# Kernel tuning notes

Measured on AMD Instinct MI355X. Metric: run time of the kernel, lower is better.

The kernel has to match this reference:

```python
import math
import jax, jax.numpy as jnp
import numpy as np

B, T, S = 4, 1024, 1024
D, H, V = 512, 8, 32000
DK = D // H
PAD_ID = 0


def _layernorm(x, g, b, eps=1e-5):
    mu = jnp.mean(x, axis=-1, keepdims=True)
    var = jnp.mean((x - mu) ** 2, axis=-1, keepdims=True)
    return g * (x - mu) / jnp.sqrt(var + eps) + b


def _pos_encoding(t, d, dtype):
    pos = jnp.arange(t, dtype=jnp.float32)[:, None]
    freqs = 1.0 / (10000.0 ** (jnp.arange(0, d, 2, dtype=jnp.float32) / d))
    pe = jnp.zeros((t, d), jnp.float32)
    pe = pe.at[:, 0::2].set(jnp.sin(pos * freqs))
    pe = pe.at[:, 1::2].set(jnp.cos(pos * freqs))
    return pe.astype(dtype)


def _split_heads(x):  # [B,L,D] -> [B,H,L,DK]
    b, l, _ = x.shape
    return x.reshape(b, l, H, DK).transpose(0, 2, 1, 3)


def _merge_heads(x):  # [B,H,L,DK] -> [B,L,D]
    b, h, l, dk = x.shape
    return x.transpose(0, 2, 1, 3).reshape(b, l, h * dk)


def _attn(q, k, v, mask):  # mask True = blocked, broadcastable to [B,H,Tq,Tk]
    s = jnp.einsum('bhqd,bhkd->bhqk', q, k) / math.sqrt(DK)
    s = jnp.where(mask, jnp.finfo(s.dtype).min, s)
    a = jax.nn.softmax(s, axis=-1)
    return jnp.einsum('bhqk,bhkd->bhqd', a, v)


def setup_inputs() -> dict:
    key = jax.random.key(0)
    ks = iter(jax.random.split(key, 40))
    def W(o, i):
        return jax.random.normal(next(ks), (o, i), jnp.float32) * 0.02
    def bvec(o):
        return jnp.zeros((o,), jnp.float32)
    inp = {
        'tokens': jax.random.randint(next(ks), (B, T), 0, V),
        'enc_embeddings': jax.random.normal(next(ks), (B, S, D), jnp.float32),
        'enc_pad_mask': jnp.zeros((B, S), bool),
        'emb': jax.random.normal(next(ks), (V, D), jnp.float32) * 0.02,
        'Wq': W(D, D), 'bq': bvec(D), 'Wk': W(D, D), 'bk': bvec(D),
        'Wv': W(D, D), 'bv': bvec(D), 'Wo1': W(D, D), 'bo1': bvec(D),
        'cWq': W(D, D), 'cbq': bvec(D), 'eWk': W(D, D), 'ebk': bvec(D),
        'eWv': W(D, D), 'ebv': bvec(D), 'Wo2': W(D, D), 'bo2': bvec(D),
        'W1': W(2 * D, D), 'b1': bvec(2 * D), 'W2': W(D, 2 * D), 'b2': bvec(D),
        'g1': jnp.ones((D,), jnp.float32), 'be1': bvec(D),
        'g2': jnp.ones((D,), jnp.float32), 'be2': bvec(D),
        'g3': jnp.ones((D,), jnp.float32), 'be3': bvec(D),
        'Wout': W(V, D), 'bout': bvec(V),
    }
    return inp


def reference(tokens, enc_embeddings, enc_pad_mask, emb,
              Wq, bq, Wk, bk, Wv, bv, Wo1, bo1,
              cWq, cbq, eWk, ebk, eWv, ebv, Wo2, bo2,
              W1, b1, W2, b2, g1, be1, g2, be2, g3, be3, Wout, bout):
    lin = lambda x, w, b: x @ w.T + b
    x = emb[tokens] * math.sqrt(D)                      # [B,T,D]
    x = x + _pos_encoding(T, D, x.dtype)[None]
    # causal self-attention with key-padding mask
    q = _split_heads(lin(x, Wq, bq))
    k = _split_heads(lin(x, Wk, bk))
    v = _split_heads(lin(x, Wv, bv))
    causal = jnp.arange(T)[None, :] > jnp.arange(T)[:, None]          # [T,T]
    key_pad = (tokens == PAD_ID)[:, None, None, :]                    # [B,1,1,T]
    sa = _merge_heads(_attn(q, k, v, causal[None, None] | key_pad))
    x = _layernorm(lin(sa, Wo1, bo1) + x, g1, be1)
    # cross-attention
    dq = _split_heads(lin(x, cWq, cbq))
    ek = _split_heads(lin(enc_embeddings, eWk, ebk))
    ev = _split_heads(lin(enc_embeddings, eWv, ebv))
    ca = _merge_heads(_attn(dq, ek, ev, enc_pad_mask[:, None, None, :]))
    x = _layernorm(lin(ca, Wo2, bo2) + x, g3, be3)
    # FFN
    fp = lin(jax.nn.relu(lin(x, W1, b1)), W2, b2)
    x = _layernorm(x + fp, g2, be2)
    return lin(x, Wout, bout)                            # [B,T,V]
```

## Files before the change

### kernel.cpp

```cpp
#include <hip/hip_runtime.h>

#define DEV __device__ __forceinline__

typedef unsigned short u16;
typedef __attribute__((ext_vector_type(8))) __bf16 bf16x8;
typedef __attribute__((ext_vector_type(4))) float f32x4;

DEV u16 f2b(float f) {
    unsigned u = __builtin_bit_cast(unsigned, f);
    unsigned r = u + 0x7fffu + ((u >> 16) & 1u);
    return (u16)(r >> 16);
}

DEV f32x4 mfma16(bf16x8 a, bf16x8 b, f32x4 c) {
    return __builtin_amdgcn_mfma_f32_16x16x32_bf16(a, b, c, 0, 0, 0);
}

#define GLOAD_LDS16(gp, lp)                                                       \
    __builtin_amdgcn_global_load_lds((__attribute__((address_space(1))) void*)(gp), \
                                     (__attribute__((address_space(3))) void*)(lp), \
                                     16, 0, 0)

template <int L>
DEV void wait_ring(int kt, int NT) {
    if (kt + 2 < NT) {
        if constexpr (L == 2) asm volatile("s_waitcnt vmcnt(4)" ::: "memory");
        if constexpr (L == 3) asm volatile("s_waitcnt vmcnt(6)" ::: "memory");
        if constexpr (L == 4) asm volatile("s_waitcnt vmcnt(8)" ::: "memory");
    } else if (kt + 1 < NT) {
        if constexpr (L == 2) asm volatile("s_waitcnt vmcnt(2)" ::: "memory");
        if constexpr (L == 3) asm volatile("s_waitcnt vmcnt(3)" ::: "memory");
        if constexpr (L == 4) asm volatile("s_waitcnt vmcnt(4)" ::: "memory");
    } else {
        asm volatile("s_waitcnt vmcnt(0)" ::: "memory");
    }
}

struct CastArgs {
    const float4* src[12];
    ushort4* dst[12];
    int start4[13];
    const int* tokens;
    const float* emb;
    float* xf;
    u16* xb;
};

__global__ __launch_bounds__(256) void cast_embed_k(CastArgs a) {
    const int bid = blockIdx.x;
    if (bid < 4096) {
        int i   = bid * 256 + threadIdx.x;
        int row = i >> 8;
        int dp  = i & 255;
        int pos = row & 1023;
        int tok = a.tokens[row];
        const float* e = a.emb + (size_t)tok * 512 + dp * 2;
        float e0 = e[0] * 22.627416997969522f;
        float e1 = e[1] * 22.627416997969522f;
        float freq = exp2f(-(float)dp * 0.05190512648262190f);
        float ang  = (float)pos * freq;
        float v0 = e0 + __sinf(ang);
        float v1 = e1 + __cosf(ang);
        size_t o = (size_t)row * 512 + dp * 2;
        a.xf[o] = v0; a.xf[o + 1] = v1;
        a.xb[o] = f2b(v0); a.xb[o + 1] = f2b(v1);
        return;
    }
    const int total = a.start4[12];
    const int nblk = gridDim.x - 4096;
    for (int i = (bid - 4096) * 256 + threadIdx.x; i < total; i += nblk * 256) {
        int j = 0;
#pragma unroll
        for (int t = 1; t < 12; t++) j += (i >= a.start4[t]) ? 1 : 0;
        const int loc = i - a.start4[j];
        float4 v = a.src[j][loc];
        ushort4 o;
        o.x = f2b(v.x); o.y = f2b(v.y); o.z = f2b(v.z); o.w = f2b(v.w);
        a.dst[j][loc] = o;
    }
}

template <int BM, int BN>
__global__ __launch_bounds__(256) void gemm_sm_k(const u16* __restrict__ A,
                                                 const u16* __restrict__ W,
                                                 const float* __restrict__ b0,
                                                 const float* __restrict__ b1,
                                                 const float* __restrict__ b2,
                                                 float* __restrict__ Cf,
                                                 u16* __restrict__ Cb,
                                                 int M, int N, int K, int relu) {
    constexpr int MF = BM / 32;
    constexpr int NF = BN / 32;
    constexpr int CH_A = BM * 4;
    constexpr int CH_TOT = (BM + BN) * 4;
    constexpr int L = CH_TOT / 256;
    __shared__ u16 sA[4][BM * 32];
    __shared__ u16 sB[4][BN * 32];

    const int gx = gridDim.x;
    const int nwg = gx * gridDim.y;
    const int orig = blockIdx.y * gx + blockIdx.x;
    const int xcd = orig & 7, chnk = orig >> 3;
    const int q = nwg >> 3, r = nwg & 7;
    const int wgid = (xcd < r ? xcd * (q + 1) : r * (q + 1) + (xcd - r) * q) + chnk;
    const int m0 = (wgid % gx) * BM;
    const int n0 = (wgid / gx) * BN;

    const int tid  = threadIdx.x;
    const int lane = tid & 63;
    const int wid  = tid >> 6;
    const int wr = wid >> 1, wc = wid & 1;
    const int lg = lane >> 4, lr = lane & 15;

    f32x4 acc[MF][NF];
#pragma unroll
    for (int i = 0; i < MF; i++)
#pragma unroll
        for (int j = 0; j < NF; j++) acc[i][j] = (f32x4){0.f, 0.f, 0.f, 0.f};

    auto stage = [&](int b, int kt) {
        const int k0 = kt << 5;
#pragma unroll
        for (int h = 0; h < L; h++) {
            const int c = tid + h * 256;
            if (c < CH_A) {
                const int row = c >> 2, ch = c & 3;
                const int gch = ch ^ ((row >> 1) & 3);
                GLOAD_LDS16(A + (size_t)(m0 + row) * K + k0 + gch * 8,
                            &sA[b][c * 8]);
            } else {
                const int cb = c - CH_A;
                const int row = cb >> 2, ch = cb & 3;
                const int gch = ch ^ ((row >> 1) & 3);
                GLOAD_LDS16(W + (size_t)(n0 + row) * K + k0 + gch * 8,
                            &sB[b][cb * 8]);
            }
        }
    };

    const int NT = K >> 5;
    stage(0, 0); stage(1, 1); stage(2, 2);

    for (int kt = 0; kt < NT; kt++) {
        wait_ring<L>(kt, NT);
        __builtin_amdgcn_s_barrier();
        const int bsel = kt & 3;
        if (kt + 3 < NT) stage((kt + 3) & 3, kt + 3);

        bf16x8 af[MF], bfr[NF];
#pragma unroll
        for (int mi = 0; mi < MF; mi++) {
            const int row = wr * (BM / 2) + mi * 16 + lr;
            af[mi] = *(const bf16x8*)(&sA[bsel][row * 32 + (lg ^ ((row >> 1) & 3)) * 8]);
        }
#pragma unroll
        for (int ni = 0; ni < NF; ni++) {
            const int row = wc * (BN / 2) + ni * 16 + lr;
            bfr[ni] = *(const bf16x8*)(&sB[bsel][row * 32 + (lg ^ ((row >> 1) & 3)) * 8]);
        }
        __builtin_amdgcn_s_setprio(1);
#pragma unroll
        for (int mi = 0; mi < MF; mi++)
#pragma unroll
            for (int ni = 0; ni < NF; ni++)
                acc[mi][ni] = mfma16(af[mi], bfr[ni], acc[mi][ni]);
        __builtin_amdgcn_s_setprio(0);
    }

#pragma unroll
    for (int mi = 0; mi < MF; mi++) {
        const int rbase = m0 + wr * (BM / 2) + mi * 16 + lg * 4;
#pragma unroll
        for (int ni = 0; ni < NF; ni++) {
            const int col = n0 + wc * (BN / 2) + ni * 16 + lr;
            const float* bp = b0; int cc = col;
            if (b1 && col >= 512)  { bp = b1; cc = col - 512; }
            if (b2 && col >= 1024) { bp = b2; cc = col - 1024; }
            const float bv = bp[cc];
#pragma unroll
            for (int rr = 0; rr < 4; rr++) {
                float v = acc[mi][ni][rr] + bv;
                if (relu) v = fmaxf(v, 0.f);
                if (Cf) Cf[(size_t)(rbase + rr) * N + col] = v;
                if (Cb) Cb[(size_t)(rbase + rr) * N + col] = f2b(v);
            }
        }
    }
}

__global__ __launch_bounds__(256) void gemm_wout_k(const u16* __restrict__ A,
                                                   const u16* __restrict__ W,
                                                   const float* __restrict__ bias,
                                                   float* __restrict__ C,
                                                   int M, int N, int K) {
    __shared__ u16 sA[2][128 * 32];
    __shared__ u16 sB[2][128 * 32];
    const int orig = blockIdx.x;
    const int wgid = (orig & 7) * (8000 / 8) + (orig >> 3);
    const int m0 = (wgid & 31) * 128;
    const int n0 = (wgid >> 5) * 128;

    const int tid  = threadIdx.x;
    const int lane = tid & 63;
    const int wid  = tid >> 6;
    const int wr = wid >> 1, wc = wid & 1;
    const int lg = lane >> 4, lr = lane & 15;

    f32x4 acc[4][4];
#pragma unroll
    for (int i = 0; i < 4; i++)
#pragma unroll
        for (int j = 0; j < 4; j++) acc[i][j] = (f32x4){0.f, 0.f, 0.f, 0.f};

    auto stage = [&](int b, int kt) {
        const int k0 = kt << 5;
#pragma unroll
        for (int h = 0; h < 4; h++) {
            const int c = tid + h * 256;
            if (c < 512) {
                const int row = c >> 2, ch = c & 3;
                const int gch = ch ^ ((row >> 1) & 3);
                GLOAD_LDS16(A + (size_t)(m0 + row) * K + k0 + gch * 8,
                            &sA[b][c * 8]);
            } else {
                const int cb = c - 512;
                const int row = cb >> 2, ch = cb & 3;
                const int gch = ch ^ ((row >> 1) & 3);
                GLOAD_LDS16(W + (size_t)(n0 + row) * K + k0 + gch * 8,
                            &sB[b][cb * 8]);
            }
        }
    };

    const int NT = K >> 5;
    stage(0, 0);
    for (int kt = 0; kt < NT; kt++) {
        asm volatile("s_waitcnt vmcnt(0)" ::: "memory");
        __builtin_amdgcn_s_barrier();
        const int bsel = kt & 1;
        if (kt + 1 < NT) stage(bsel ^ 1, kt + 1);

        bf16x8 af[4], bfr[4];
#pragma unroll
        for (int mi = 0; mi < 4; mi++) {
            const int row = wr * 64 + mi * 16 + lr;
            af[mi] = *(const bf16x8*)(&sA[bsel][row * 32 + (lg ^ ((row >> 1) & 3)) * 8]);
        }
#pragma unroll
        for (int ni = 0; ni < 4; ni++) {
            const int row = wc * 64 + ni * 16 + lr;
            bfr[ni] = *(const bf16x8*)(&sB[bsel][row * 32 + (lg ^ ((row >> 1) & 3)) * 8]);
        }
        __builtin_amdgcn_s_setprio(1);
#pragma unroll
        for (int mi = 0; mi < 4; mi++)
#pragma unroll
            for (int ni = 0; ni < 4; ni++)
                acc[mi][ni] = mfma16(af[mi], bfr[ni], acc[mi][ni]);
        __builtin_amdgcn_s_setprio(0);
    }

#pragma unroll
    for (int mi = 0; mi < 4; mi++) {
        const int rbase = m0 + wr * 64 + mi * 16 + lg * 4;
#pragma unroll
        for (int ni = 0; ni < 4; ni++) {
            const int col = n0 + wc * 64 + ni * 16 + lr;
            const float bv = bias[col];
#pragma unroll
            for (int rr = 0; rr < 4; rr++)
                __builtin_nontemporal_store(acc[mi][ni][rr] + bv,
                                            &C[(size_t)(rbase + rr) * N + col]);
        }
    }
}

struct DualArgs {
    const u16 *A0, *W0, *A1, *W1;
    const float *b00, *b01, *b02, *b10, *b11;
    u16 *C0, *C1;
};

__global__ __launch_bounds__(256) void gemm_dual_k(DualArgs da) {
    constexpr int BM = 64, BN = 128, MF = 2, NF = 4;
    constexpr int CH_A = BM * 4, CH_TOT = (BM + BN) * 4, L = CH_TOT / 256;
    __shared__ u16 sA[4][BM * 32];
    __shared__ u16 sB[4][BN * 32];

    const int z = blockIdx.z;
    const int gy = z ? 8 : 12;
    if ((int)blockIdx.y >= gy) return;
    const int N = z ? 1024 : 1536;
    const u16* A = z ? da.A1 : da.A0;
    const u16* W = z ? da.W1 : da.W0;
    u16* C = z ? da.C1 : da.C0;
    const int K = 512;

    const int gx = gridDim.x;
    const int nwg = gx * gy;
    const int orig = blockIdx.y * gx + blockIdx.x;
    const int xcd = orig & 7, chnk = orig >> 3;
    const int q = nwg >> 3, r = nwg & 7;
    const int wgid = (xcd < r ? xcd * (q + 1) : r * (q + 1) + (xcd - r) * q) + chnk;
    const int m0 = (wgid % gx) * BM;
    const int n0 = (wgid / gx) * BN;

    const int tid  = threadIdx.x;
    const int lane = tid & 63;
    const int wid  = tid >> 6;
    const int wr = wid >> 1, wc = wid & 1;
    const int lg = lane >> 4, lr = lane & 15;

    f32x4 acc[MF][NF];
#pragma unroll
    for (int i = 0; i < MF; i++)
#pragma unroll
        for (int j = 0; j < NF; j++) acc[i][j] = (f32x4){0.f, 0.f, 0.f, 0.f};

    auto stage = [&](int b, int kt) {
        const int k0 = kt << 5;
#pragma unroll
        for (int h = 0; h < L; h++) {
            const int c = tid + h * 256;
            if (c < CH_A) {
                const int row = c >> 2, ch = c & 3;
                const int gch = ch ^ ((row >> 1) & 3);
                GLOAD_LDS16(A + (size_t)(m0 + row) * K + k0 + gch * 8,
                            &sA[b][c * 8]);
            } else {
                const int cb = c - CH_A;
                const int row = cb >> 2, ch = cb & 3;
                const int gch = ch ^ ((row >> 1) & 3);
                GLOAD_LDS16(W + (size_t)(n0 + row) * K + k0 + gch * 8,
                            &sB[b][cb * 8]);
            }
        }
    };

    const int NT = K >> 5;
    stage(0, 0); stage(1, 1); stage(2, 2);

    for (int kt = 0; kt < NT; kt++) {
        wait_ring<L>(kt, NT);
        __builtin_amdgcn_s_barrier();
        const int bsel = kt & 3;
        if (kt + 3 < NT) stage((kt + 3) & 3, kt + 3);

        bf16x8 af[MF], bfr[NF];
#pragma unroll
        for (int mi = 0; mi < MF; mi++) {
            const int row = wr * (BM / 2) + mi * 16 + lr;
            af[mi] = *(const bf16x8*)(&sA[bsel][row * 32 + (lg ^ ((row >> 1) & 3)) * 8]);
        }
#pragma unroll
        for (int ni = 0; ni < NF; ni++) {
            const int row = wc * (BN / 2) + ni * 16 + lr;
            bfr[ni] = *(const bf16x8*)(&sB[bsel][row * 32 + (lg ^ ((row >> 1) & 3)) * 8]);
        }
        __builtin_amdgcn_s_setprio(1);
#pragma unroll
        for (int mi = 0; mi < MF; mi++)
#pragma unroll
            for (int ni = 0; ni < NF; ni++)
                acc[mi][ni] = mfma16(af[mi], bfr[ni], acc[mi][ni]);
        __builtin_amdgcn_s_setprio(0);
    }

#pragma unroll
    for (int mi = 0; mi < MF; mi++) {
        const int rbase = m0 + wr * (BM / 2) + mi * 16 + lg * 4;
#pragma unroll
        for (int ni = 0; ni < NF; ni++) {
            const int col = n0 + wc * (BN / 2) + ni * 16 + lr;
            const float* bp; int cc;
            if (z == 0) {
                if (col >= 1024)     { bp = da.b02; cc = col - 1024; }
                else if (col >= 512) { bp = da.b01; cc = col - 512; }
                else                 { bp = da.b00; cc = col; }
            } else {
                if (col >= 512)      { bp = da.b11; cc = col - 512; }
                else                 { bp = da.b10; cc = col; }
            }
            const float bv = bp[cc];
#pragma unroll
            for (int rr = 0; rr < 4; rr++)
                C[(size_t)(rbase + rr) * N + col] = f2b(acc[mi][ni][rr] + bv);
        }
    }
}

__global__ __launch_bounds__(256) void vt_k(const u16* __restrict__ V0, int rs0,
                                            u16* __restrict__ VT0,
                                            const u16* __restrict__ V1, int rs1,
                                            u16* __restrict__ VT1) {
    const u16* V = blockIdx.z ? V1 : V0;
    u16* VT = blockIdx.z ? VT1 : VT0;
    const int rs = blockIdx.z ? rs1 : rs0;
    const int bh = blockIdx.x;
    const int b = bh >> 3;
    const int h64 = (bh & 7) * 64;
    const int t0 = blockIdx.y * 64;
    __shared__ u16 s[64 * 65];
    const int tid = threadIdx.x;
#pragma unroll
    for (int i = 0; i < 16; i++) {
        int t = (tid >> 6) + i * 4;
        int d = tid & 63;
        s[d * 65 + t] = V[(size_t)(b * 1024 + t0 + t) * rs + h64 + d];
    }
    __syncthreads();
#pragma unroll
    for (int i = 0; i < 16; i++) {
        int d = (tid >> 6) + i * 4;
        int t = tid & 63;
        VT[(size_t)(bh * 64 + d) * 1024 + t0 + t] = s[d * 65 + t];
    }
}

template <int CAUSAL>
__global__ __launch_bounds__(64) void attn_k(const u16* __restrict__ Q, int qrs,
                                             const u16* __restrict__ Kb, int krs,
                                             const u16* __restrict__ VT,
                                             const int* __restrict__ tokens,
                                             const signed char* __restrict__ km8,
                                             u16* __restrict__ O, int LK) {
    const int bh = blockIdx.x;
    const int b = bh >> 3;
    const int h64 = (bh & 7) * 64;
    const int qb = blockIdx.y;
    const int lane = threadIdx.x;
    const int lg = lane >> 4, lr = lane & 15;
    const float NEG = -3.402823466e38f;

    const u16* qrow = Q + (size_t)(b * 1024 + qb * 16 + lr) * qrs + h64 + lg * 8;
    const bf16x8 aq0 = *(const bf16x8*)(qrow);
    const bf16x8 aq1 = *(const bf16x8*)(qrow + 32);

    f32x4 o[4];
#pragma unroll
    for (int ni = 0; ni < 4; ni++) o[ni] = (f32x4){0.f, 0.f, 0.f, 0.f};
    float m_run[4], l_run[4];
#pragma unroll
    for (int rr = 0; rr < 4; rr++) { m_run[rr] = NEG; l_run[rr] = 0.f; }

    __shared__ u16 sP[16 * 72];
    const u16* vbase = VT + (size_t)bh * 64 * LK;

    auto body = [&](int k0) {
        f32x4 s[4];
#pragma unroll
        for (int c = 0; c < 4; c++) {
            const u16* krow =
                Kb + (size_t)(b * LK + k0 + c * 16 + lr) * krs + h64 + lg * 8;
            bf16x8 bk0 = *(const bf16x8*)(krow);
            bf16x8 bk1 = *(const bf16x8*)(krow + 32);
            f32x4 t = (f32x4){0.f, 0.f, 0.f, 0.f};
            t = mfma16(aq0, bk0, t);
            t = mfma16(aq1, bk1, t);
            s[c] = t;
        }
#pragma unroll
        for (int c = 0; c < 4; c++) {
            const int key = k0 + c * 16 + lr;
            bool mkey;
            if (CAUSAL) mkey = (tokens[b * LK + key] == 0);
            else        mkey = (km8[b * LK + key] != 0);
#pragma unroll
            for (int rr = 0; rr < 4; rr++) {
                float sv = s[c][rr] * 0.125f;
                bool mk = mkey;
                if (CAUSAL) mk = mk || (key > qb * 16 + lg * 4 + rr);
                s[c][rr] = mk ? NEG : sv;
            }
        }
        float pf[4];
#pragma unroll
        for (int rr = 0; rr < 4; rr++) {
            float bm = fmaxf(fmaxf(s[0][rr], s[1][rr]), fmaxf(s[2][rr], s[3][rr]));
            bm = fmaxf(bm, __shfl_xor(bm, 1));
            bm = fmaxf(bm, __shfl_xor(bm, 2));
            bm = fmaxf(bm, __shfl_xor(bm, 4));
            bm = fmaxf(bm, __shfl_xor(bm, 8));
            float mn = fmaxf(m_run[rr], bm);
            float sc = __expf(m_run[rr] - mn);
            float p0 = __expf(s[0][rr] - mn);
            float p1 = __expf(s[1][rr] - mn);
            float p2 = __expf(s[2][rr] - mn);
            float p3 = __expf(s[3][rr] - mn);
            float bs = (p0 + p1) + (p2 + p3);
            bs += __shfl_xor(bs, 1);
            bs += __shfl_xor(bs, 2);
            bs += __shfl_xor(bs, 4);
            bs += __shfl_xor(bs, 8);
            l_run[rr] = l_run[rr] * sc + bs;
            m_run[rr] = mn;
            pf[rr] = sc;
            s[0][rr] = p0; s[1][rr] = p1; s[2][rr] = p2; s[3][rr] = p3;
        }
#pragma unroll
        for (int ni = 0; ni < 4; ni++)
#pragma unroll
            for (int rr = 0; rr < 4; rr++) o[ni][rr] *= pf[rr];
        __syncthreads();
#pragma unroll
        for (int c = 0; c < 4; c++)
#pragma unroll
            for (int rr = 0; rr < 4; rr++)
                sP[(lg * 4 + rr) * 72 + c * 16 + lr] = f2b(s[c][rr]);
        __syncthreads();
        bf16x8 ap0 = *(const bf16x8*)(sP + lr * 72 + lg * 8);
        bf16x8 ap1 = *(const bf16x8*)(sP + lr * 72 + 32 + lg * 8);
#pragma unroll
        for (int ni = 0; ni < 4; ni++) {
            const u16* vrow = vbase + (size_t)(ni * 16 + lr) * LK + k0 + lg * 8;
            bf16x8 bv0 = *(const bf16x8*)(vrow);
            bf16x8 bv1 = *(const bf16x8*)(vrow + 32);
            o[ni] = mfma16(ap0, bv0, o[ni]);
            o[ni] = mfma16(ap1, bv1, o[ni]);
        }
    };

    int kend = CAUSAL ? ((((qb * 16 + 15) >> 6) + 1) << 6) : LK;
    if (kend > LK) kend = LK;
    for (int k0 = 0; k0 < kend; k0 += 64) body(k0);
    if (CAUSAL && kend < LK) {
        bool fm = (m_run[0] == NEG) || (m_run[1] == NEG) ||
                  (m_run[2] == NEG) || (m_run[3] == NEG);
        if (__any(fm))
            for (int k0 = kend; k0 < LK; k0 += 64) body(k0);
    }

#pragma unroll
    for (int ni = 0; ni < 4; ni++)
#pragma unroll
        for (int rr = 0; rr < 4; rr++) {
            float v = o[ni][rr] / l_run[rr];
            O[(size_t)(b * 1024 + qb * 16 + lg * 4 + rr) * 512 + h64 + ni * 16 + lr] =
                f2b(v);
        }
}

__global__ __launch_bounds__(256) void ln_k(const float* __restrict__ a,
                                            const float* __restrict__ res,
                                            const float* __restrict__ g,
                                            const float* __restrict__ be,
                                            float* __restrict__ outf,
                                            u16* __restrict__ outb) {
    const int row = blockIdx.x;
    const int tid = threadIdx.x;
    const size_t base = (size_t)row * 512;
    float2 av = ((const float2*)(a + base))[tid];
    float2 rv = ((const float2*)(res + base))[tid];
    float x0 = av.x + rv.x;
    float x1 = av.y + rv.y;
    float s = x0 + x1, q = x0 * x0 + x1 * x1;
#pragma unroll
    for (int off = 1; off < 64; off <<= 1) {
        s += __shfl_xor(s, off);
        q += __shfl_xor(q, off);
    }
    __shared__ float ps[8];
    const int wid = tid >> 6;
    if ((tid & 63) == 0) { ps[wid] = s; ps[wid + 4] = q; }
    __syncthreads();
    s = ps[0] + ps[1] + ps[2] + ps[3];
    q = ps[4] + ps[5] + ps[6] + ps[7];
    const float mu = s * (1.f / 512.f);
    const float var = q * (1.f / 512.f) - mu * mu;
    const float inv = rsqrtf(var + 1e-5f);
    float2 gv = ((const float2*)g)[tid];
    float2 bv = ((const float2*)be)[tid];
    float y0 = gv.x * (x0 - mu) * inv + bv.x;
    float y1 = gv.y * (x1 - mu) * inv + bv.y;
    if (outf) { ((float2*)(outf + base))[tid] = make_float2(y0, y1); }
    outb[base + tid * 2] = f2b(y0);
    outb[base + tid * 2 + 1] = f2b(y1);
}

extern "C" void kernel_launch(void* const* d_in, const int* in_sizes, int n_in,
                              void* d_out, int out_size, void* d_ws, size_t ws_size,
                              hipStream_t stream) {
    (void)in_sizes; (void)n_in; (void)out_size;
    const int*   tokens  = (const int*)d_in[0];
    const float* enc     = (const float*)d_in[1];
    const signed char* encmask = (const signed char*)d_in[2];
    const float* emb     = (const float*)d_in[3];
    const float* Wq  = (const float*)d_in[4];  const float* bq  = (const float*)d_in[5];
    const float* Wk  = (const float*)d_in[6];  const float* bk  = (const float*)d_in[7];
    const float* Wv  = (const float*)d_in[8];  const float* bv  = (const float*)d_in[9];
    const float* Wo1 = (const float*)d_in[10]; const float* bo1 = (const float*)d_in[11];
    const float* cWq = (const float*)d_in[12]; const float* cbq = (const float*)d_in[13];
    const float* eWk = (const float*)d_in[14]; const float* ebk = (const float*)d_in[15];
    const float* eWv = (const float*)d_in[16]; const float* ebv = (const float*)d_in[17];
    const float* Wo2 = (const float*)d_in[18]; const float* bo2 = (const float*)d_in[19];
    const float* W1  = (const float*)d_in[20]; const float* b1  = (const float*)d_in[21];
    const float* W2  = (const float*)d_in[22]; const float* b2  = (const float*)d_in[23];
    const float* g1  = (const float*)d_in[24]; const float* be1 = (const float*)d_in[25];
    const float* g2  = (const float*)d_in[26]; const float* be2 = (const float*)d_in[27];
    const float* g3  = (const float*)d_in[28]; const float* be3 = (const float*)d_in[29];
    const float* Wout= (const float*)d_in[30]; const float* bout= (const float*)d_in[31];
    float* out = (float*)d_out;

    char* ws = (char*)d_ws;
    size_t off = 0;
    auto alloc = [&](size_t bytes) -> void* {
        void* p = ws + off;
        off += (bytes + 255) & ~(size_t)255;
        return p;
    };

    u16* Wqkvb = (u16*)alloc((size_t)786432 * 2);
    u16* Wo1b  = (u16*)alloc(262144 * 2);
    u16* cWqb  = (u16*)alloc(262144 * 2);
    u16* eWkvb = (u16*)alloc((size_t)524288 * 2);
    u16* Wo2b  = (u16*)alloc(262144 * 2);
    u16* W1b   = (u16*)alloc(524288 * 2);
    u16* W2b   = (u16*)alloc(524288 * 2);
    u16* Woutb = (u16*)alloc((size_t)16384000 * 2);
    u16* encb  = (u16*)alloc((size_t)2097152 * 2);
    float* x0f = (float*)alloc((size_t)2097152 * 4);
    u16*   x0b = (u16*)alloc((size_t)2097152 * 2);
    float* x1f = (float*)alloc((size_t)2097152 * 4);
    u16*   x1b = (u16*)alloc((size_t)2097152 * 2);
    float* x2f = (float*)alloc((size_t)2097152 * 4);
    u16*   x2b = (u16*)alloc((size_t)2097152 * 2);
    u16*   x3b = (u16*)alloc((size_t)2097152 * 2);
    u16* qkv = (u16*)alloc((size_t)4096 * 1536 * 2);
    u16* ekv = (u16*)alloc((size_t)4096 * 1024 * 2);
    u16* cq  = (u16*)alloc((size_t)2097152 * 2);
    u16* vt  = (u16*)alloc((size_t)2097152 * 2);
    u16* vt2 = (u16*)alloc((size_t)2097152 * 2);
    u16* t4  = (u16*)alloc((size_t)2097152 * 2);
    float* p8 = (float*)alloc((size_t)2097152 * 4);
    u16*  hb  = (u16*)alloc((size_t)4194304 * 2);
    if (off > ws_size) return;

    CastArgs ca;
    const float* srcs[12] = {Wq, Wk, Wv, Wo1, cWq, eWk, eWv, Wo2, W1, W2, enc, Wout};
    u16* dsts[12] = {Wqkvb, Wqkvb + 262144, Wqkvb + 524288, Wo1b, cWqb,
                     eWkvb, eWkvb + 262144, Wo2b, W1b, W2b, encb, Woutb};
    int ns[12] = {262144, 262144, 262144, 262144, 262144, 262144, 262144, 262144,
                  524288, 524288, 2097152, 16384000};
    int acc4 = 0;
    for (int j = 0; j < 12; j++) {
        ca.src[j] = (const float4*)srcs[j];
        ca.dst[j] = (ushort4*)dsts[j];
        ca.start4[j] = acc4;
        acc4 += ns[j] / 4;
    }
    ca.start4[12] = acc4;
    ca.tokens = tokens; ca.emb = emb; ca.xf = x0f; ca.xb = x0b;
    cast_embed_k<<<4096 + 2048, 256, 0, stream>>>(ca);

    DualArgs da;
    da.A0 = x0b;  da.W0 = Wqkvb; da.A1 = encb; da.W1 = eWkvb;
    da.b00 = bq;  da.b01 = bk;   da.b02 = bv;
    da.b10 = ebk; da.b11 = ebv;
    da.C0 = qkv;  da.C1 = ekv;
    gemm_dual_k<<<dim3(64, 12, 2), 256, 0, stream>>>(da);

    vt_k<<<dim3(32, 16, 2), 256, 0, stream>>>(qkv + 1024, 1536, vt,
                                              ekv + 512, 1024, vt2);

    attn_k<1><<<dim3(32, 64), 64, 0, stream>>>(qkv, 1536, qkv + 512, 1536, vt,
                                               tokens, nullptr, t4, 1024);
    gemm_sm_k<64, 64><<<dim3(64, 8), 256, 0, stream>>>(
        t4, Wo1b, bo1, nullptr, nullptr, p8, nullptr, 4096, 512, 512, 0);
    ln_k<<<4096, 256, 0, stream>>>(p8, x0f, g1, be1, x1f, x1b);

    gemm_sm_k<64, 64><<<dim3(64, 8), 256, 0, stream>>>(
        x1b, cWqb, cbq, nullptr, nullptr, nullptr, cq, 4096, 512, 512, 0);
    attn_k<0><<<dim3(32, 64), 64, 0, stream>>>(cq, 512, ekv, 1024, vt2,
                                               nullptr, encmask, t4, 1024);
    gemm_sm_k<64, 64><<<dim3(64, 8), 256, 0, stream>>>(
        t4, Wo2b, bo2, nullptr, nullptr, p8, nullptr, 4096, 512, 512, 0);
    ln_k<<<4096, 256, 0, stream>>>(p8, x1f, g3, be3, x2f, x2b);

    gemm_sm_k<64, 128><<<dim3(64, 8), 256, 0, stream>>>(
        x2b, W1b, b1, nullptr, nullptr, nullptr, hb, 4096, 1024, 512, 1);
    gemm_sm_k<64, 64><<<dim3(64, 8), 256, 0, stream>>>(
        hb, W2b, b2, nullptr, nullptr, p8, nullptr, 4096, 512, 1024, 0);
    ln_k<<<4096, 256, 0, stream>>>(p8, x2f, g2, be2, nullptr, x3b);

    gemm_wout_k<<<8000, 256, 0, stream>>>(x3b, Woutb, bout, out, 4096, 32000, 512);
}
```

Measured before the change: 470.8 us.

## Process 32 queries per attention wave and regroup Wout tile order

The attention kernel now handles two 16-row query groups per 64-thread block, so each loaded K and V fragment feeds twice as many MFMAs and half as many blocks are launched. Separately, the Wout GEMM block-to-tile mapping is changed to 8x5 groups of tiles so that neighbouring workgroups share A and W tiles in cache. The attention change doubles register use for accumulators and scores, and halves the grid, which may reduce occupancy. Causal blocks also coarsen to 32-row granularity.

```diff
diff --git a/kernel.cpp b/kernel.cpp
--- a/kernel.cpp
+++ b/kernel.cpp
@@ -196,9 +196,10 @@
     __shared__ u16 sA[2][128 * 32];
     __shared__ u16 sB[2][128 * 32];
     const int orig = blockIdx.x;
-    const int wgid = (orig & 7) * (8000 / 8) + (orig >> 3);
-    const int m0 = (wgid & 31) * 128;
-    const int n0 = (wgid >> 5) * 128;
+    const int wgid = (orig & 7) * 1000 + (orig >> 3);
+    const int g = wgid / 40, w = wgid % 40;
+    const int m0 = ((g & 3) * 8 + (w & 7)) * 128;
+    const int n0 = ((g >> 2) * 5 + (w >> 3)) * 128;
 
     const int tid  = threadIdx.x;
     const int lane = tid & 63;
@@ -432,32 +433,44 @@
     const int lg = lane >> 4, lr = lane & 15;
     const float NEG = -3.402823466e38f;
 
-    const u16* qrow = Q + (size_t)(b * 1024 + qb * 16 + lr) * qrs + h64 + lg * 8;
-    const bf16x8 aq0 = *(const bf16x8*)(qrow);
-    const bf16x8 aq1 = *(const bf16x8*)(qrow + 32);
-
-    f32x4 o[4];
-#pragma unroll
-    for (int ni = 0; ni < 4; ni++) o[ni] = (f32x4){0.f, 0.f, 0.f, 0.f};
-    float m_run[4], l_run[4];
-#pragma unroll
-    for (int rr = 0; rr < 4; rr++) { m_run[rr] = NEG; l_run[rr] = 0.f; }
-
-    __shared__ u16 sP[16 * 72];
+    bf16x8 aq[2][2];
+#pragma unroll
+    for (int gq = 0; gq < 2; gq++) {
+        const u16* qrow =
+            Q + (size_t)(b * 1024 + qb * 32 + gq * 16 + lr) * qrs + h64 + lg * 8;
+        aq[gq][0] = *(const bf16x8*)(qrow);
+        aq[gq][1] = *(const bf16x8*)(qrow + 32);
+    }
+
+    f32x4 o[2][4];
+#pragma unroll
+    for (int gq = 0; gq < 2; gq++)
+#pragma unroll
+        for (int ni = 0; ni < 4; ni++) o[gq][ni] = (f32x4){0.f, 0.f, 0.f, 0.f};
+    float m_run[2][4], l_run[2][4];
+#pragma unroll
+    for (int gq = 0; gq < 2; gq++)
+#pragma unroll
+        for (int rr = 0; rr < 4; rr++) { m_run[gq][rr] = NEG; l_run[gq][rr] = 0.f; }
+
+    __shared__ u16 sP[32 * 72];
     const u16* vbase = VT + (size_t)bh * 64 * LK;
 
     auto body = [&](int k0) {
-        f32x4 s[4];
+        f32x4 s[2][4];
 #pragma unroll
         for (int c = 0; c < 4; c++) {
             const u16* krow =
                 Kb + (size_t)(b * LK + k0 + c * 16 + lr) * krs + h64 + lg * 8;
             bf16x8 bk0 = *(const bf16x8*)(krow);
             bf16x8 bk1 = *(const bf16x8*)(krow + 32);
-            f32x4 t = (f32x4){0.f, 0.f, 0.f, 0.f};
-            t = mfma16(aq0, bk0, t);
-            t = mfma16(aq1, bk1, t);
-            s[c] = t;
+#pragma unroll
+            for (int gq = 0; gq < 2; gq++) {
+                f32x4 t = (f32x4){0.f, 0.f, 0.f, 0.f};
+                t = mfma16(aq[gq][0], bk0, t);
+                t = mfma16(aq[gq][1], bk1, t);
+                s[gq][c] = t;
+            }
         }
 #pragma unroll
         for (int c = 0; c < 4; c++) {
@@ -466,78 +479,101 @@
             if (CAUSAL) mkey = (tokens[b * LK + key] == 0);
             else        mkey = (km8[b * LK + key] != 0);
 #pragma unroll
+            for (int gq = 0; gq < 2; gq++)
+#pragma unroll
+                for (int rr = 0; rr < 4; rr++) {
+                    float sv = s[gq][c][rr] * 0.125f;
+                    bool mk = mkey;
+                    if (CAUSAL)
+                        mk = mk || (key > qb * 32 + gq * 16 + lg * 4 + rr);
+                    s[gq][c][rr] = mk ? NEG : sv;
+                }
+        }
+#pragma unroll
+        for (int gq = 0; gq < 2; gq++) {
+            float pf[4];
+#pragma unroll
             for (int rr = 0; rr < 4; rr++) {
-                float sv = s[c][rr] * 0.125f;
-                bool mk = mkey;
-                if (CAUSAL) mk = mk || (key > qb * 16 + lg * 4 + rr);
-                s[c][rr] = mk ? NEG : sv;
-            }
-        }
-        float pf[4];
-#pragma unroll
-        for (int rr = 0; rr < 4; rr++) {
-            float bm = fmaxf(fmaxf(s[0][rr], s[1][rr]), fmaxf(s[2][rr], s[3][rr]));
-            bm = fmaxf(bm, __shfl_xor(bm, 1));
-            bm = fmaxf(bm, __shfl_xor(bm, 2));
-            bm = fmaxf(bm, __shfl_xor(bm, 4));
-            bm = fmaxf(bm, __shfl_xor(bm, 8));
-            float mn = fmaxf(m_run[rr], bm);
-            float sc = __expf(m_run[rr] - mn);
-            float p0 = __expf(s[0][rr] - mn);
-            float p1 = __expf(s[1][rr] - mn);
-            float p2 = __expf(s[2][rr] - mn);
-            float p3 = __expf(s[3][rr] - mn);
-            float bs = (p0 + p1) + (p2 + p3);
-            bs += __shfl_xor(bs, 1);
-            bs += __shfl_xor(bs, 2);
-            bs += __shfl_xor(bs, 4);
-            bs += __shfl_xor(bs, 8);
-            l_run[rr] = l_run[rr] * sc + bs;
-            m_run[rr] = mn;
-            pf[rr] = sc;
-            s[0][rr] = p0; s[1][rr] = p1; s[2][rr] = p2; s[3][rr] = p3;
-        }
-#pragma unroll
-        for (int ni = 0; ni < 4; ni++)
-#pragma unroll
-            for (int rr = 0; rr < 4; rr++) o[ni][rr] *= pf[rr];
+                float bm = fmaxf(fmaxf(s[gq][0][rr], s[gq][1][rr]),
+                                 fmaxf(s[gq][2][rr], s[gq][3][rr]));
+                bm = fmaxf(bm, __shfl_xor(bm, 1));
+                bm = fmaxf(bm, __shfl_xor(bm, 2));
+                bm = fmaxf(bm, __shfl_xor(bm, 4));
+                bm = fmaxf(bm, __shfl_xor(bm, 8));
+                float mn = fmaxf(m_run[gq][rr], bm);
+                float sc = __expf(m_run[gq][rr] - mn);
+                float p0 = __expf(s[gq][0][rr] - mn);
+                float p1 = __expf(s[gq][1][rr] - mn);
+                float p2 = __expf(s[gq][2][rr] - mn);
+                float p3 = __expf(s[gq][3][rr] - mn);
+                float bs = (p0 + p1) + (p2 + p3);
+                bs += __shfl_xor(bs, 1);
+                bs += __shfl_xor(bs, 2);
+                bs += __shfl_xor(bs, 4);
+                bs += __shfl_xor(bs, 8);
+                l_run[gq][rr] = l_run[gq][rr] * sc + bs;
+                m_run[gq][rr] = mn;
+                pf[rr] = sc;
+                s[gq][0][rr] = p0; s[gq][1][rr] = p1;
+                s[gq][2][rr] = p2; s[gq][3][rr] = p3;
+            }
+#pragma unroll
+            for (int ni = 0; ni < 4; ni++)
+#pragma unroll
+                for (int rr = 0; rr < 4; rr++) o[gq][ni][rr] *= pf[rr];
+        }
         __syncthreads();
 #pragma unroll
-        for (int c = 0; c < 4; c++)
-#pragma unroll
-            for (int rr = 0; rr < 4; rr++)
-                sP[(lg * 4 + rr) * 72 + c * 16 + lr] = f2b(s[c][rr]);
+        for (int gq = 0; gq < 2; gq++)
+#pragma unroll
+            for (int c = 0; c < 4; c++)
+#pragma unroll
+                for (int rr = 0; rr < 4; rr++)
+                    sP[(gq * 16 + lg * 4 + rr) * 72 + c * 16 + lr] =
+                        f2b(s[gq][c][rr]);
         __syncthreads();
-        bf16x8 ap0 = *(const bf16x8*)(sP + lr * 72 + lg * 8);
-        bf16x8 ap1 = *(const bf16x8*)(sP + lr * 72 + 32 + lg * 8);
+        bf16x8 ap[2][2];
+#pragma unroll
+        for (int gq = 0; gq < 2; gq++) {
+            ap[gq][0] = *(const bf16x8*)(sP + (gq * 16 + lr) * 72 + lg * 8);
+            ap[gq][1] = *(const bf16x8*)(sP + (gq * 16 + lr) * 72 + 32 + lg * 8);
+        }
 #pragma unroll
         for (int ni = 0; ni < 4; ni++) {
             const u16* vrow = vbase + (size_t)(ni * 16 + lr) * LK + k0 + lg * 8;
             bf16x8 bv0 = *(const bf16x8*)(vrow);
             bf16x8 bv1 = *(const bf16x8*)(vrow + 32);
-            o[ni] = mfma16(ap0, bv0, o[ni]);
-            o[ni] = mfma16(ap1, bv1, o[ni]);
+#pragma unroll
+            for (int gq = 0; gq < 2; gq++) {
+                o[gq][ni] = mfma16(ap[gq][0], bv0, o[gq][ni]);
+                o[gq][ni] = mfma16(ap[gq][1], bv1, o[gq][ni]);
+            }
         }
     };
 
-    int kend = CAUSAL ? ((((qb * 16 + 15) >> 6) + 1) << 6) : LK;
+    int kend = CAUSAL ? ((((qb * 32 + 31) >> 6) + 1) << 6) : LK;
     if (kend > LK) kend = LK;
     for (int k0 = 0; k0 < kend; k0 += 64) body(k0);
     if (CAUSAL && kend < LK) {
-        bool fm = (m_run[0] == NEG) || (m_run[1] == NEG) ||
-                  (m_run[2] == NEG) || (m_run[3] == NEG);
+        bool fm = false;
+#pragma unroll
+        for (int gq = 0; gq < 2; gq++)
+#pragma unroll
+            for (int rr = 0; rr < 4; rr++) fm = fm || (m_run[gq][rr] == NEG);
         if (__any(fm))
             for (int k0 = kend; k0 < LK; k0 += 64) body(k0);
     }
 
 #pragma unroll
-    for (int ni = 0; ni < 4; ni++)
-#pragma unroll
-        for (int rr = 0; rr < 4; rr++) {
-            float v = o[ni][rr] / l_run[rr];
-            O[(size_t)(b * 1024 + qb * 16 + lg * 4 + rr) * 512 + h64 + ni * 16 + lr] =
-                f2b(v);
-        }
+    for (int gq = 0; gq < 2; gq++)
+#pragma unroll
+        for (int ni = 0; ni < 4; ni++)
+#pragma unroll
+            for (int rr = 0; rr < 4; rr++) {
+                float v = o[gq][ni][rr] / l_run[gq][rr];
+                O[(size_t)(b * 1024 + qb * 32 + gq * 16 + lg * 4 + rr) * 512 +
+                  h64 + ni * 16 + lr] = f2b(v);
+            }
 }
 
 __global__ __launch_bounds__(256) void ln_k(const float* __restrict__ a,
@@ -662,7 +698,7 @@
     vt_k<<<dim3(32, 16, 2), 256, 0, stream>>>(qkv + 1024, 1536, vt,
                                               ekv + 512, 1024, vt2);
 
-    attn_k<1><<<dim3(32, 64), 64, 0, stream>>>(qkv, 1536, qkv + 512, 1536, vt,
+    attn_k<1><<<dim3(32, 32), 64, 0, stream>>>(qkv, 1536, qkv + 512, 1536, vt,
                                                tokens, nullptr, t4, 1024);
     gemm_sm_k<64, 64><<<dim3(64, 8), 256, 0, stream>>>(
         t4, Wo1b, bo1, nullptr, nullptr, p8, nullptr, 4096, 512, 512, 0);
@@ -670,7 +706,7 @@
 
     gemm_sm_k<64, 64><<<dim3(64, 8), 256, 0, stream>>>(
         x1b, cWqb, cbq, nullptr, nullptr, nullptr, cq, 4096, 512, 512, 0);
-    attn_k<0><<<dim3(32, 64), 64, 0, stream>>>(cq, 512, ekv, 1024, vt2,
+    attn_k<0><<<dim3(32, 32), 64, 0, stream>>>(cq, 512, ekv, 1024, vt2,
                                                nullptr, encmask, t4, 1024);
     gemm_sm_k<64, 64><<<dim3(64, 8), 256, 0, stream>>>(
         t4, Wo2b, bo2, nullptr, nullptr, p8, nullptr, 4096, 512, 512, 0);
```

After: 526.9 us. 1.12x slower.

## Share K/V tiles across four waves in attention via double-buffered LDS staging

Applied to the files above, without the earlier changes.

The attention kernel moves from one 64-thread wave per 16-query block to a 256-thread block covering 64 queries. K and V^T tiles are staged once per block into swizzled, double-buffered shared memory with direct global-to-LDS loads, so four waves reuse them instead of each reading global memory separately. Per-wave P buffers remove block-wide barriers inside the body, and s_setprio is placed around the MFMA sections. The trade-offs are coarser causal skipping (64-query granularity), a block-wide barrier every iteration, and fewer, larger blocks.

```diff
diff --git a/kernel.cpp b/kernel.cpp
--- a/kernel.cpp
+++ b/kernel.cpp
@@ -196,7 +196,7 @@
     __shared__ u16 sA[2][128 * 32];
     __shared__ u16 sB[2][128 * 32];
     const int orig = blockIdx.x;
-    const int wgid = (orig & 7) * (8000 / 8) + (orig >> 3);
+    const int wgid = (orig & 7) * 1000 + (orig >> 3);
     const int m0 = (wgid & 31) * 128;
     const int n0 = (wgid >> 5) * 128;
 
@@ -418,21 +418,29 @@
 }
 
 template <int CAUSAL>
-__global__ __launch_bounds__(64) void attn_k(const u16* __restrict__ Q, int qrs,
-                                             const u16* __restrict__ Kb, int krs,
-                                             const u16* __restrict__ VT,
-                                             const int* __restrict__ tokens,
-                                             const signed char* __restrict__ km8,
-                                             u16* __restrict__ O, int LK) {
+__global__ __launch_bounds__(256) void attn_k(const u16* __restrict__ Q, int qrs,
+                                              const u16* __restrict__ Kb, int krs,
+                                              const u16* __restrict__ VT,
+                                              const int* __restrict__ tokens,
+                                              const signed char* __restrict__ km8,
+                                              u16* __restrict__ O, int LK) {
     const int bh = blockIdx.x;
     const int b = bh >> 3;
     const int h64 = (bh & 7) * 64;
-    const int qb = blockIdx.y;
-    const int lane = threadIdx.x;
+    const int qblk = blockIdx.y;
+    const int tid = threadIdx.x;
+    const int wid = tid >> 6;
+    const int lane = tid & 63;
     const int lg = lane >> 4, lr = lane & 15;
     const float NEG = -3.402823466e38f;
 
-    const u16* qrow = Q + (size_t)(b * 1024 + qb * 16 + lr) * qrs + h64 + lg * 8;
+    __shared__ u16 sK[2][64 * 64];
+    __shared__ u16 sV[2][64 * 64];
+    __shared__ u16 sP[4][16 * 72];
+    __shared__ int sFlag;
+
+    const int q0 = qblk * 64 + wid * 16;
+    const u16* qrow = Q + (size_t)(b * 1024 + q0 + lr) * qrs + h64 + lg * 8;
     const bf16x8 aq0 = *(const bf16x8*)(qrow);
     const bf16x8 aq1 = *(const bf16x8*)(qrow + 32);
 
@@ -443,22 +451,41 @@
 #pragma unroll
     for (int rr = 0; rr < 4; rr++) { m_run[rr] = NEG; l_run[rr] = 0.f; }
 
-    __shared__ u16 sP[16 * 72];
+    const u16* kbase = Kb + (size_t)b * LK * krs + h64;
     const u16* vbase = VT + (size_t)bh * 64 * LK;
 
-    auto body = [&](int k0) {
+    auto stage = [&](int buf, int k0) {
+#pragma unroll
+        for (int h = 0; h < 2; h++) {
+            const int cidx = tid + h * 256;
+            const int rk = cidx >> 3, ch = cidx & 7;
+            GLOAD_LDS16(kbase + (size_t)(k0 + rk) * krs + (ch ^ (rk & 7)) * 8,
+                        &sK[buf][cidx * 8]);
+        }
+#pragma unroll
+        for (int h = 0; h < 2; h++) {
+            const int cidx = tid + h * 256;
+            const int dv = cidx >> 3, ch = cidx & 7;
+            GLOAD_LDS16(vbase + (size_t)dv * LK + k0 + (ch ^ (dv & 7)) * 8,
+                        &sV[buf][cidx * 8]);
+        }
+    };
+
+    auto body = [&](int cur, int k0) {
         f32x4 s[4];
+        __builtin_amdgcn_s_setprio(1);
 #pragma unroll
         for (int c = 0; c < 4; c++) {
-            const u16* krow =
-                Kb + (size_t)(b * LK + k0 + c * 16 + lr) * krs + h64 + lg * 8;
-            bf16x8 bk0 = *(const bf16x8*)(krow);
-            bf16x8 bk1 = *(const bf16x8*)(krow + 32);
+            const int rk = c * 16 + lr;
+            bf16x8 bk0 = *(const bf16x8*)(&sK[cur][(rk * 8 + (lg ^ (rk & 7))) * 8]);
+            bf16x8 bk1 =
+                *(const bf16x8*)(&sK[cur][(rk * 8 + ((lg + 4) ^ (rk & 7))) * 8]);
             f32x4 t = (f32x4){0.f, 0.f, 0.f, 0.f};
             t = mfma16(aq0, bk0, t);
             t = mfma16(aq1, bk1, t);
             s[c] = t;
         }
+        __builtin_amdgcn_s_setprio(0);
 #pragma unroll
         for (int c = 0; c < 4; c++) {
             const int key = k0 + c * 16 + lr;
@@ -469,7 +496,7 @@
             for (int rr = 0; rr < 4; rr++) {
                 float sv = s[c][rr] * 0.125f;
                 bool mk = mkey;
-                if (CAUSAL) mk = mk || (key > qb * 16 + lg * 4 + rr);
+                if (CAUSAL) mk = mk || (key > q0 + lg * 4 + rr);
                 s[c][rr] = mk ? NEG : sv;
             }
         }
@@ -501,33 +528,55 @@
         for (int ni = 0; ni < 4; ni++)
 #pragma unroll
             for (int rr = 0; rr < 4; rr++) o[ni][rr] *= pf[rr];
-        __syncthreads();
 #pragma unroll
         for (int c = 0; c < 4; c++)
 #pragma unroll
             for (int rr = 0; rr < 4; rr++)
-                sP[(lg * 4 + rr) * 72 + c * 16 + lr] = f2b(s[c][rr]);
-        __syncthreads();
-        bf16x8 ap0 = *(const bf16x8*)(sP + lr * 72 + lg * 8);
-        bf16x8 ap1 = *(const bf16x8*)(sP + lr * 72 + 32 + lg * 8);
+                sP[wid][(lg * 4 + rr) * 72 + c * 16 + lr] = f2b(s[c][rr]);
+        bf16x8 ap0 = *(const bf16x8*)(&sP[wid][lr * 72 + lg * 8]);
+        bf16x8 ap1 = *(const bf16x8*)(&sP[wid][lr * 72 + 32 + lg * 8]);
+        __builtin_amdgcn_s_setprio(1);
 #pragma unroll
         for (int ni = 0; ni < 4; ni++) {
-            const u16* vrow = vbase + (size_t)(ni * 16 + lr) * LK + k0 + lg * 8;
-            bf16x8 bv0 = *(const bf16x8*)(vrow);
-            bf16x8 bv1 = *(const bf16x8*)(vrow + 32);
+            const int rv = ni * 16 + lr;
+            bf16x8 bv0 = *(const bf16x8*)(&sV[cur][(rv * 8 + (lg ^ (rv & 7))) * 8]);
+            bf16x8 bv1 =
+                *(const bf16x8*)(&sV[cur][(rv * 8 + ((lg + 4) ^ (rv & 7))) * 8]);
             o[ni] = mfma16(ap0, bv0, o[ni]);
             o[ni] = mfma16(ap1, bv1, o[ni]);
         }
+        __builtin_amdgcn_s_setprio(0);
     };
 
-    int kend = CAUSAL ? ((((qb * 16 + 15) >> 6) + 1) << 6) : LK;
+    int kend = CAUSAL ? ((qblk + 1) << 6) : LK;
     if (kend > LK) kend = LK;
-    for (int k0 = 0; k0 < kend; k0 += 64) body(k0);
+    const int nit = kend >> 6;
+    stage(0, 0);
+    for (int it = 0; it < nit; it++) {
+        asm volatile("s_waitcnt vmcnt(0)" ::: "memory");
+        __syncthreads();
+        const int cur = it & 1;
+        if (it + 1 < nit) stage(cur ^ 1, (it + 1) << 6);
+        body(cur, it << 6);
+    }
     if (CAUSAL && kend < LK) {
         bool fm = (m_run[0] == NEG) || (m_run[1] == NEG) ||
                   (m_run[2] == NEG) || (m_run[3] == NEG);
-        if (__any(fm))
-            for (int k0 = kend; k0 < LK; k0 += 64) body(k0);
+        if (tid == 0) sFlag = 0;
+        __syncthreads();
+        if (__any(fm) && lane == 0) sFlag = 1;
+        __syncthreads();
+        if (sFlag) {
+            const int nit2 = LK >> 6;
+            stage(nit & 1, nit << 6);
+            for (int it = nit; it < nit2; it++) {
+                asm volatile("s_waitcnt vmcnt(0)" ::: "memory");
+                __syncthreads();
+                const int cur = it & 1;
+                if (it + 1 < nit2) stage(cur ^ 1, (it + 1) << 6);
+                body(cur, it << 6);
+            }
+        }
     }
 
 #pragma unroll
@@ -535,7 +584,7 @@
 #pragma unroll
         for (int rr = 0; rr < 4; rr++) {
             float v = o[ni][rr] / l_run[rr];
-            O[(size_t)(b * 1024 + qb * 16 + lg * 4 + rr) * 512 + h64 + ni * 16 + lr] =
+            O[(size_t)(b * 1024 + q0 + lg * 4 + rr) * 512 + h64 + ni * 16 + lr] =
                 f2b(v);
         }
 }
@@ -662,16 +711,16 @@
     vt_k<<<dim3(32, 16, 2), 256, 0, stream>>>(qkv + 1024, 1536, vt,
                                               ekv + 512, 1024, vt2);
 
-    attn_k<1><<<dim3(32, 64), 64, 0, stream>>>(qkv, 1536, qkv + 512, 1536, vt,
-                                               tokens, nullptr, t4, 1024);
+    attn_k<1><<<dim3(32, 16), 256, 0, stream>>>(qkv, 1536, qkv + 512, 1536, vt,
+                                                tokens, nullptr, t4, 1024);
     gemm_sm_k<64, 64><<<dim3(64, 8), 256, 0, stream>>>(
         t4, Wo1b, bo1, nullptr, nullptr, p8, nullptr, 4096, 512, 512, 0);
     ln_k<<<4096, 256, 0, stream>>>(p8, x0f, g1, be1, x1f, x1b);
 
     gemm_sm_k<64, 64><<<dim3(64, 8), 256, 0, stream>>>(
         x1b, cWqb, cbq, nullptr, nullptr, nullptr, cq, 4096, 512, 512, 0);
-    attn_k<0><<<dim3(32, 64), 64, 0, stream>>>(cq, 512, ekv, 1024, vt2,
-                                               nullptr, encmask, t4, 1024);
+    attn_k<0><<<dim3(32, 16), 256, 0, stream>>>(cq, 512, ekv, 1024, vt2,
+                                                nullptr, encmask, t4, 1024);
     gemm_sm_k<64, 64><<<dim3(64, 8), 256, 0, stream>>>(
         t4, Wo2b, bo2, nullptr, nullptr, p8, nullptr, 4096, 512, 512, 0);
     ln_k<<<4096, 256, 0, stream>>>(p8, x1f, g3, be3, x2f, x2b);
```

Result: faster. 411.9 us (-12.5%).
